# Kernel tuning notes

Hardware: AMD Instinct MI355X
Metric: run time of the kernel (lower is better)

## Reference

```python
import jax, jax.numpy as jnp
import numpy as np

N_PTS = 1048576
N_FEATS = 32
GRID = (96, 96, 96)
L = 6                      # num_positional_encoding_terms
D_IN = N_FEATS + 2 * L * 3  # 68
H_DIM = 128
VMIN, VMAX = -1.0, 1.0


def setup_inputs() -> dict:
    key = jax.random.key(0)
    ks = jax.random.split(key, 5)
    def lin(k, shp, fan):
        return jax.random.normal(k, shp, jnp.float32) * (1.0 / np.sqrt(fan).astype(np.float32))
    return {
        "x": jax.random.uniform(ks[0], (N_PTS, 3), jnp.float32),          # coords in [0,1) subset of [-1,1]
        "feature_grid": jax.random.uniform(ks[1], (1, N_FEATS) + GRID, jnp.float32),
        "W0": lin(ks[2], (H_DIM, D_IN), D_IN), "b0": jnp.zeros((H_DIM,), jnp.float32),
        "W1": lin(ks[3], (H_DIM, H_DIM), H_DIM), "b1": jnp.zeros((H_DIM,), jnp.float32),
        "W2": lin(ks[4], (1, H_DIM), H_DIM), "b2": jnp.zeros((1,), jnp.float32),
    }


def positional_encoding(x):
    # x: [N, d] -> [N, 2*L*d], NeRF-style: per frequency 2^i * pi, [sin | cos]
    freqs = jnp.pi * (2.0 ** jnp.arange(L, dtype=jnp.float32))   # [L]
    xf = x[:, None, :] * freqs[None, :, None]                    # [N, L, d]
    return jnp.concatenate([jnp.sin(xf), jnp.cos(xf)], axis=-1).reshape(x.shape[0], -1)


def grid_sample_3d(grid, coords):
    # Trilinear F.grid_sample, align_corners=True.
    # grid: [C, D, H, W]; coords: [N, 3] in [-1,1], ordered (x, y, z) -> (W, H, D)
    C, D, H, W = grid.shape
    def unnorm(c, size):
        return (c + 1.0) * 0.5 * (size - 1)
    fx, fy, fz = unnorm(coords[:, 0], W), unnorm(coords[:, 1], H), unnorm(coords[:, 2], D)
    x0, y0, z0 = jnp.floor(fx), jnp.floor(fy), jnp.floor(fz)
    wx, wy, wz = fx - x0, fy - y0, fz - z0
    def ci(i, size):
        return jnp.clip(i.astype(jnp.int32), 0, size - 1)
    x0i, x1i = ci(x0, W), ci(x0 + 1, W)
    y0i, y1i = ci(y0, H), ci(y0 + 1, H)
    z0i, z1i = ci(z0, D), ci(z0 + 1, D)
    def g(zi, yi, xi):
        return grid[:, zi, yi, xi]   # irregular gather -> [C, N]
    return (g(z0i, y0i, x0i) * ((1 - wz) * (1 - wy) * (1 - wx))
          + g(z0i, y0i, x1i) * ((1 - wz) * (1 - wy) * wx)
          + g(z0i, y1i, x0i) * ((1 - wz) * wy * (1 - wx))
          + g(z0i, y1i, x1i) * ((1 - wz) * wy * wx)
          + g(z1i, y0i, x0i) * (wz * (1 - wy) * (1 - wx))
          + g(z1i, y0i, x1i) * (wz * (1 - wy) * wx)
          + g(z1i, y1i, x0i) * (wz * wy * (1 - wx))
          + g(z1i, y1i, x1i) * (wz * wy * wx))   # [C, N]


def reference(x, feature_grid, W0, b0, W1, b1, W2, b2):
    feats = grid_sample_3d(feature_grid[0], x).T                       # [N, C]
    h = jnp.concatenate([positional_encoding(x), feats], axis=1)       # [N, 68]
    h = jax.nn.relu(h @ W0.T + b0)                                     # [N, 128]
    h = jax.nn.relu(h @ W1.T + b1)                                     # [N, 128]
    y = h @ W2.T + b2                                                  # [N, 1]
    return y * (VMAX - VMIN) + VMIN
```

## Files before the change

kernel.cpp:

```cpp
#include <hip/hip_runtime.h>

#define NPTS 1048576
#define NCH 32
#define GS 96
#define GV (GS * GS * GS)
#define DIN 68
#define HD 128
#define TILE_PTS 32
#define NTILES (NPTS / TILE_PTS)
#define NBLK 256
#define NTHR 768
#define WAVES_TOT (NBLK * 12)

typedef __bf16 bf16x8 __attribute__((ext_vector_type(8)));
typedef float f32x4 __attribute__((ext_vector_type(4)));
typedef float f32x2 __attribute__((ext_vector_type(2)));

__device__ __forceinline__ unsigned int f2bf(float f) {
  unsigned int u = __float_as_uint(f);
  return (u + 0x7fffu + ((u >> 16) & 1u)) >> 16;
}
__device__ __forceinline__ unsigned int pkbf(float a, float b) {
  return f2bf(a) | (f2bf(b) << 16);
}

__global__ __launch_bounds__(256) void k_prep_grid(const float* __restrict__ src,
                                                   unsigned int* __restrict__ dst) {
  __shared__ unsigned int tile[256 * 17];
  const int tid = threadIdx.x;
  const long vb = (long)blockIdx.x * 256;
  const int c2 = tid >> 4;
  const int vgb = tid & 15;
#pragma unroll
  for (int p = 0; p < 4; ++p) {
    int vox = (vgb + p * 16) * 4;
    const float4 a = *(const float4*)(src + (long)(2 * c2) * GV + vb + vox);
    const float4 b = *(const float4*)(src + (long)(2 * c2 + 1) * GV + vb + vox);
    tile[(vox + 0) * 17 + c2] = pkbf(a.x, b.x);
    tile[(vox + 1) * 17 + c2] = pkbf(a.y, b.y);
    tile[(vox + 2) * 17 + c2] = pkbf(a.z, b.z);
    tile[(vox + 3) * 17 + c2] = pkbf(a.w, b.w);
  }
  __syncthreads();
  const int vox2 = tid >> 2;
  const int c4 = (tid & 3) * 4;
#pragma unroll
  for (int j = 0; j < 4; ++j) {
    int vx = vox2 + j * 64;
    uint4 w;
    w.x = tile[vx * 17 + c4 + 0];
    w.y = tile[vx * 17 + c4 + 1];
    w.z = tile[vx * 17 + c4 + 2];
    w.w = tile[vx * 17 + c4 + 3];
    *(uint4*)(dst + (vb + vx) * 16 + c4) = w;
  }
}

template <bool TA>
__global__ __launch_bounds__(NTHR, 3) void k_fvsrn(
    const float* __restrict__ X, const float* __restrict__ gridF,
    const unsigned short* __restrict__ gridT,
    const float* __restrict__ W0, const float* __restrict__ B0,
    const float* __restrict__ W1, const float* __restrict__ B1,
    const float* __restrict__ W2, const float* __restrict__ B2,
    float* __restrict__ out) {
  extern __shared__ char smem[];
  float* lb0 = (float*)(smem + 57344);
  float* lb1 = (float*)(smem + 57856);
  float* lw2 = (float*)(smem + 58368);
  const int tid = threadIdx.x;

  for (int idx = tid; idx < 56 * 64; idx += NTHR) {
    int f = idx >> 6;
    int L = idx & 63;
    int qq = L >> 4, lnn = L & 15;
    float vals[8];
    if (f < 24) {
      int kt = f >> 3, nt = f & 7;
      int n = nt * 16 + lnn;
      int kb = kt * 32 + qq * 8;
#pragma unroll
      for (int j = 0; j < 8; ++j) {
        int k = kb + j;
        float w = 0.f;
        if (k < 32) w = W0[n * DIN + 36 + k];
        else if (k < DIN) w = W0[n * DIN + (k - 32)];
        vals[j] = w;
      }
    } else {
      int g = f - 24;
      int kt = g >> 3, nt = g & 7;
      int n = nt * 16 + lnn;
      int kb = kt * 32 + qq * 8;
#pragma unroll
      for (int j = 0; j < 8; ++j) vals[j] = W1[n * HD + kb + j];
    }
    uint4 pk;
    pk.x = pkbf(vals[0], vals[1]);
    pk.y = pkbf(vals[2], vals[3]);
    pk.z = pkbf(vals[4], vals[5]);
    pk.w = pkbf(vals[6], vals[7]);
    *(uint4*)(smem + f * 1024 + L * 16) = pk;
  }
  if (tid < 128) lb0[tid] = B0[tid];
  else if (tid < 256) lb1[tid - 128] = B1[tid - 128];
  else if (tid < 384) lw2[tid - 256] = W2[tid - 256];
  __syncthreads();

  const int wave = tid >> 6, lane = tid & 63;
  char* scr = smem + 58880 + wave * 8192;
  const int q = lane >> 4, ln = lane & 15;
  const int half = lane >> 5, pt = lane & 31;
  const int mtg = pt >> 4, pmg = pt & 15;
  const float b2s = B2[0];

  int t = blockIdx.x * 12 + wave;
  float px = 0.f, py = 0.f, pz = 0.f;
  if (t < NTILES) {
    long p = (long)t * TILE_PTS + pt;
    px = X[p * 3 + 0]; py = X[p * 3 + 1]; pz = X[p * 3 + 2];
  }

  for (; t < NTILES;) {
    const int tn = t + WAVES_TOT;
    const long p0 = (long)t * TILE_PTS;

    float v36[36];
    {
      const float PIf = 3.14159265358979f;
      float cc[3] = {px, py, pz};
#pragma unroll
      for (int ax = 0; ax < 3; ++ax) {
        float s, co;
        __sincosf(PIf * cc[ax], &s, &co);
#pragma unroll
        for (int i = 0; i < 6; ++i) {
          v36[i * 6 + ax] = s;
          v36[i * 6 + 3 + ax] = co;
          float s2 = 2.f * s * co;
          co = 1.f - 2.f * s * s;
          s = s2;
        }
      }
    }
    unsigned int pd[8], e0, e1;
    if (half == 0) {
#pragma unroll
      for (int d = 0; d < 8; ++d) pd[d] = pkbf(v36[2 * d], v36[2 * d + 1]);
      e0 = pkbf(v36[32], v36[33]);
      e1 = pkbf(v36[34], v36[35]);
    } else {
#pragma unroll
      for (int d = 0; d < 8; ++d) pd[d] = pkbf(v36[16 + 2 * d], v36[17 + 2 * d]);
      e0 = 0u; e1 = 0u;
    }

    f32x2 f2[8];
#pragma unroll
    for (int i = 0; i < 8; ++i) f2[i] = (f32x2){0.f, 0.f};
    {
      float fx = (px + 1.f) * 0.5f * (GS - 1);
      float fy = (py + 1.f) * 0.5f * (GS - 1);
      float fz = (pz + 1.f) * 0.5f * (GS - 1);
      float flx = floorf(fx), fly = floorf(fy), flz = floorf(fz);
      float wx = fx - flx, wy = fy - fly, wz = fz - flz;
      int jx = (int)flx, jy = (int)fly, jz = (int)flz;
      int ixa0 = min(max(jx, 0), GS - 1), ixa1 = min(max(jx + 1, 0), GS - 1);
      int iya0 = min(max(jy, 0), GS - 1), iya1 = min(max(jy + 1, 0), GS - 1);
      int iza0 = min(max(jz, 0), GS - 1), iza1 = min(max(jz + 1, 0), GS - 1);
#pragma unroll
      for (int zi = 0; zi < 2; ++zi) {
        int izz = zi ? iza1 : iza0;
        float wzz = zi ? wz : 1.f - wz;
#pragma unroll
        for (int yi = 0; yi < 2; ++yi) {
          int iyy = yi ? iya1 : iya0;
          float wyy = yi ? wy : 1.f - wy;
#pragma unroll
          for (int xi = 0; xi < 2; ++xi) {
            int ixx = xi ? ixa1 : ixa0;
            float w = wzz * wyy * (xi ? wx : 1.f - wx);
            f32x2 w2 = {w, w};
            long vi = ((long)izz * GS + iyy) * GS + ixx;
            if constexpr (TA) {
              const uint4* gp = (const uint4*)(gridT + vi * NCH + 16 * half);
              uint4 g0 = gp[0], g1 = gp[1];
#define ACC_PAIR(u, i)                                                     \
  {                                                                        \
    f32x2 u2 = {__uint_as_float((u) << 16),                                \
                __uint_as_float((u) & 0xffff0000u)};                       \
    f2[i] = __builtin_elementwise_fma(u2, w2, f2[i]);                      \
  }
              ACC_PAIR(g0.x, 0) ACC_PAIR(g0.y, 1) ACC_PAIR(g0.z, 2) ACC_PAIR(g0.w, 3)
              ACC_PAIR(g1.x, 4) ACC_PAIR(g1.y, 5) ACC_PAIR(g1.z, 6) ACC_PAIR(g1.w, 7)
#undef ACC_PAIR
            } else {
#pragma unroll
              for (int i = 0; i < 8; ++i) {
                int c = 16 * half + 2 * i;
                f32x2 u2 = {gridF[(long)c * GV + vi], gridF[(long)(c + 1) * GV + vi]};
                f2[i] = __builtin_elementwise_fma(u2, w2, f2[i]);
              }
            }
          }
        }
      }
    }

    {
      char* fbase = scr + (mtg * 3) * 1024;
      int ro = pmg * 16;
      uint4 s;
      s.x = pkbf(f2[0].x, f2[0].y); s.y = pkbf(f2[1].x, f2[1].y);
      s.z = pkbf(f2[2].x, f2[2].y); s.w = pkbf(f2[3].x, f2[3].y);
      *(uint4*)(fbase + (2 * half) * 256 + ro) = s;
      s.x = pkbf(f2[4].x, f2[4].y); s.y = pkbf(f2[5].x, f2[5].y);
      s.z = pkbf(f2[6].x, f2[6].y); s.w = pkbf(f2[7].x, f2[7].y);
      *(uint4*)(fbase + (2 * half + 1) * 256 + ro) = s;
      s.x = pd[0]; s.y = pd[1]; s.z = pd[2]; s.w = pd[3];
      *(uint4*)(fbase + 1024 + (2 * half) * 256 + ro) = s;
      s.x = pd[4]; s.y = pd[5]; s.z = pd[6]; s.w = pd[7];
      *(uint4*)(fbase + 1024 + (2 * half + 1) * 256 + ro) = s;
      s.x = e0; s.y = e1; s.z = 0u; s.w = 0u;
      *(uint4*)(fbase + 2048 + (2 * half) * 256 + ro) = s;
      s.x = 0u; s.y = 0u; s.z = 0u; s.w = 0u;
      *(uint4*)(fbase + 2048 + (2 * half + 1) * 256 + ro) = s;
    }
    __builtin_amdgcn_wave_barrier();

    if (tn < NTILES) {
      long p = (long)tn * TILE_PTS + pt;
      px = X[p * 3 + 0]; py = X[p * 3 + 1]; pz = X[p * 3 + 2];
    }

    bf16x8 a0[6];
#pragma unroll
    for (int mt = 0; mt < 2; ++mt)
#pragma unroll
      for (int kt = 0; kt < 3; ++kt)
        a0[mt * 3 + kt] = *(const bf16x8*)(scr + (mt * 3 + kt) * 1024 + lane * 16);
    __builtin_amdgcn_wave_barrier();
#pragma unroll
    for (int nt = 0; nt < 8; ++nt) {
      float bn = lb0[nt * 16 + ln];
      f32x4 cinit = {bn, bn, bn, bn};
      f32x4 acc[2];
      acc[0] = cinit; acc[1] = cinit;
#pragma unroll
      for (int kt = 0; kt < 3; ++kt) {
        bf16x8 bfr = *(const bf16x8*)(smem + (kt * 8 + nt) * 1024 + lane * 16);
#pragma unroll
        for (int mt = 0; mt < 2; ++mt)
          acc[mt] = __builtin_amdgcn_mfma_f32_16x16x32_bf16(a0[mt * 3 + kt], bfr, acc[mt], 0, 0, 0);
      }
      int n = nt * 16 + ln;
      int kt1 = n >> 5, j = n & 7, sub = (n >> 3) & 3;
#pragma unroll
      for (int mt = 0; mt < 2; ++mt)
#pragma unroll
        for (int r = 0; r < 4; ++r) {
          float h = fmaxf(acc[mt][r], 0.f);
          *(unsigned short*)(scr + (mt * 4 + kt1) * 1024 + (sub * 16 + q * 4 + r) * 16 + j * 2) =
              (unsigned short)f2bf(h);
        }
    }
    __builtin_amdgcn_wave_barrier();

    bf16x8 a1[8];
#pragma unroll
    for (int mt = 0; mt < 2; ++mt)
#pragma unroll
      for (int kt = 0; kt < 4; ++kt)
        a1[mt * 4 + kt] = *(const bf16x8*)(scr + (mt * 4 + kt) * 1024 + lane * 16);
    __builtin_amdgcn_wave_barrier();
    float y[8];
#pragma unroll
    for (int i = 0; i < 8; ++i) y[i] = 0.f;
#pragma unroll
    for (int nt = 0; nt < 8; ++nt) {
      float bn = lb1[nt * 16 + ln];
      float w2n = lw2[nt * 16 + ln];
      f32x4 cinit = {bn, bn, bn, bn};
      f32x4 acc[2];
      acc[0] = cinit; acc[1] = cinit;
#pragma unroll
      for (int kt = 0; kt < 4; ++kt) {
        bf16x8 bfr = *(const bf16x8*)(smem + 24576 + (kt * 8 + nt) * 1024 + lane * 16);
#pragma unroll
        for (int mt = 0; mt < 2; ++mt)
          acc[mt] = __builtin_amdgcn_mfma_f32_16x16x32_bf16(a1[mt * 4 + kt], bfr, acc[mt], 0, 0, 0);
      }
#pragma unroll
      for (int mt = 0; mt < 2; ++mt)
#pragma unroll
        for (int r = 0; r < 4; ++r)
          y[mt * 4 + r] += w2n * fmaxf(acc[mt][r], 0.f);
    }
#pragma unroll
    for (int i = 0; i < 8; ++i) {
      float v = y[i];
      v += __shfl_xor(v, 1);
      v += __shfl_xor(v, 2);
      v += __shfl_xor(v, 4);
      v += __shfl_xor(v, 8);
      y[i] = v;
    }
    if (ln == 0) {
#pragma unroll
      for (int mt = 0; mt < 2; ++mt)
#pragma unroll
        for (int r = 0; r < 4; ++r)
          out[p0 + mt * 16 + q * 4 + r] = (y[mt * 4 + r] + b2s) * 2.f - 1.f;
    }
    t = tn;
  }
}

extern "C" void kernel_launch(void* const* d_in, const int* in_sizes, int n_in,
                              void* d_out, int out_size, void* d_ws, size_t ws_size,
                              hipStream_t stream) {
  const float* X  = (const float*)d_in[0];
  const float* G  = (const float*)d_in[1];
  const float* W0 = (const float*)d_in[2];
  const float* B0 = (const float*)d_in[3];
  const float* W1 = (const float*)d_in[4];
  const float* B1 = (const float*)d_in[5];
  const float* W2 = (const float*)d_in[6];
  const float* B2 = (const float*)d_in[7];
  float* out = (float*)d_out;

  const size_t needT = (size_t)GV * NCH * 2;
  const size_t shmem = 157184;

  if (ws_size >= needT) {
    k_prep_grid<<<GV / 256, 256, 0, stream>>>(G, (unsigned int*)d_ws);
    k_fvsrn<true><<<NBLK, NTHR, shmem, stream>>>(
        X, G, (const unsigned short*)d_ws, W0, B0, W1, B1, W2, B2, out);
  } else {
    k_fvsrn<false><<<NBLK, NTHR, shmem, stream>>>(
        X, G, (const unsigned short*)nullptr, W0, B0, W1, B1, W2, B2, out);
  }
}
```

Before: 301.0 us.

## Prefetch next tile's grid corner gathers across MLP and use packed bf16 convert

Issues the eight trilinear corner gathers for the next tile into 16 uint4 registers before the current tile's MLP runs, so gather latency overlaps the MFMA work. It also loads the next coordinates earlier, uses 32-bit index arithmetic, and switches bf16 packing to a hardware packed-convert builtin when one is available, packing two ReLU outputs per convert. The cost is 64 more live VGPRs, which may lower occupancy. The initial coordinate load also loses its bounds check.

```diff
diff --git a/kernel.cpp b/kernel.cpp
--- a/kernel.cpp
+++ b/kernel.cpp
@@ -21,7 +21,11 @@
   return (u + 0x7fffu + ((u >> 16) & 1u)) >> 16;
 }
 __device__ __forceinline__ unsigned int pkbf(float a, float b) {
+#if __has_builtin(__builtin_amdgcn_cvt_pk_bf16_f32)
+  return __builtin_bit_cast(unsigned int, __builtin_amdgcn_cvt_pk_bf16_f32(a, b));
+#else
   return f2bf(a) | (f2bf(b) << 16);
+#endif
 }
 
 __global__ __launch_bounds__(256) void k_prep_grid(const float* __restrict__ src,
@@ -115,15 +119,48 @@
   const float b2s = B2[0];
 
   int t = blockIdx.x * 12 + wave;
-  float px = 0.f, py = 0.f, pz = 0.f;
-  if (t < NTILES) {
-    long p = (long)t * TILE_PTS + pt;
-    px = X[p * 3 + 0]; py = X[p * 3 + 1]; pz = X[p * 3 + 2];
-  }
+  unsigned p3 = ((unsigned)t * TILE_PTS + pt) * 3u;
+  float px = X[p3], py = X[p3 + 1], pz = X[p3 + 2];
+
+  uint4 cg[16];
+
+  auto corner_issue = [&](float cx, float cy, float cz) {
+    float fx = (cx + 1.f) * 0.5f * (GS - 1);
+    float fy = (cy + 1.f) * 0.5f * (GS - 1);
+    float fz = (cz + 1.f) * 0.5f * (GS - 1);
+    int jx = (int)floorf(fx), jy = (int)floorf(fy), jz = (int)floorf(fz);
+    int ix0 = min(max(jx, 0), GS - 1), ix1 = min(max(jx + 1, 0), GS - 1);
+    int iy0 = min(max(jy, 0), GS - 1), iy1 = min(max(jy + 1, 0), GS - 1);
+    int iz0 = min(max(jz, 0), GS - 1), iz1 = min(max(jz + 1, 0), GS - 1);
+    unsigned zy[4];
+    zy[0] = ((unsigned)(iz0 * GS + iy0)) * GS;
+    zy[1] = ((unsigned)(iz0 * GS + iy1)) * GS;
+    zy[2] = ((unsigned)(iz1 * GS + iy0)) * GS;
+    zy[3] = ((unsigned)(iz1 * GS + iy1)) * GS;
+    unsigned hb = (unsigned)(half << 4);
+#pragma unroll
+    for (int c = 0; c < 4; ++c) {
+      unsigned o0 = ((zy[c] + (unsigned)ix0) << 5) + hb;
+      unsigned o1 = ((zy[c] + (unsigned)ix1) << 5) + hb;
+      const uint4* g0 = (const uint4*)(gridT + o0);
+      const uint4* g1 = (const uint4*)(gridT + o1);
+      cg[4 * c + 0] = g0[0];
+      cg[4 * c + 1] = g0[1];
+      cg[4 * c + 2] = g1[0];
+      cg[4 * c + 3] = g1[1];
+    }
+  };
+  if constexpr (TA) corner_issue(px, py, pz);
 
   for (; t < NTILES;) {
     const int tn = t + WAVES_TOT;
-    const long p0 = (long)t * TILE_PTS;
+    const unsigned p0 = (unsigned)t * TILE_PTS;
+
+    float nx = px, ny = py, nz = pz;
+    if (tn < NTILES) {
+      unsigned np3 = ((unsigned)tn * TILE_PTS + pt) * 3u;
+      nx = X[np3]; ny = X[np3 + 1]; nz = X[np3 + 2];
+    }
 
     float v36[36];
     {
@@ -162,49 +199,52 @@
       float fx = (px + 1.f) * 0.5f * (GS - 1);
       float fy = (py + 1.f) * 0.5f * (GS - 1);
       float fz = (pz + 1.f) * 0.5f * (GS - 1);
-      float flx = floorf(fx), fly = floorf(fy), flz = floorf(fz);
-      float wx = fx - flx, wy = fy - fly, wz = fz - flz;
-      int jx = (int)flx, jy = (int)fly, jz = (int)flz;
-      int ixa0 = min(max(jx, 0), GS - 1), ixa1 = min(max(jx + 1, 0), GS - 1);
-      int iya0 = min(max(jy, 0), GS - 1), iya1 = min(max(jy + 1, 0), GS - 1);
-      int iza0 = min(max(jz, 0), GS - 1), iza1 = min(max(jz + 1, 0), GS - 1);
-#pragma unroll
-      for (int zi = 0; zi < 2; ++zi) {
-        int izz = zi ? iza1 : iza0;
-        float wzz = zi ? wz : 1.f - wz;
-#pragma unroll
-        for (int yi = 0; yi < 2; ++yi) {
-          int iyy = yi ? iya1 : iya0;
-          float wyy = yi ? wy : 1.f - wy;
-#pragma unroll
-          for (int xi = 0; xi < 2; ++xi) {
-            int ixx = xi ? ixa1 : ixa0;
-            float w = wzz * wyy * (xi ? wx : 1.f - wx);
-            f32x2 w2 = {w, w};
-            long vi = ((long)izz * GS + iyy) * GS + ixx;
-            if constexpr (TA) {
-              const uint4* gp = (const uint4*)(gridT + vi * NCH + 16 * half);
-              uint4 g0 = gp[0], g1 = gp[1];
+      float wx = fx - floorf(fx), wy = fy - floorf(fy), wz = fz - floorf(fz);
+      float wxa[2] = {1.f - wx, wx};
+      float wya[2] = {1.f - wy, wy};
+      float wza[2] = {1.f - wz, wz};
+      if constexpr (TA) {
+#pragma unroll
+        for (int c = 0; c < 8; ++c) {
+          int zi = c >> 2, yi = (c >> 1) & 1, xi = c & 1;
+          float w = wza[zi] * wya[yi] * wxa[xi];
+          f32x2 w2 = {w, w};
+          uint4 g0 = cg[4 * (zi * 2 + yi) + xi * 2 + 0];
+          uint4 g1 = cg[4 * (zi * 2 + yi) + xi * 2 + 1];
 #define ACC_PAIR(u, i)                                                     \
   {                                                                        \
     f32x2 u2 = {__uint_as_float((u) << 16),                                \
                 __uint_as_float((u) & 0xffff0000u)};                       \
     f2[i] = __builtin_elementwise_fma(u2, w2, f2[i]);                      \
   }
-              ACC_PAIR(g0.x, 0) ACC_PAIR(g0.y, 1) ACC_PAIR(g0.z, 2) ACC_PAIR(g0.w, 3)
-              ACC_PAIR(g1.x, 4) ACC_PAIR(g1.y, 5) ACC_PAIR(g1.z, 6) ACC_PAIR(g1.w, 7)
+          ACC_PAIR(g0.x, 0) ACC_PAIR(g0.y, 1) ACC_PAIR(g0.z, 2) ACC_PAIR(g0.w, 3)
+          ACC_PAIR(g1.x, 4) ACC_PAIR(g1.y, 5) ACC_PAIR(g1.z, 6) ACC_PAIR(g1.w, 7)
 #undef ACC_PAIR
-            } else {
-#pragma unroll
-              for (int i = 0; i < 8; ++i) {
-                int c = 16 * half + 2 * i;
-                f32x2 u2 = {gridF[(long)c * GV + vi], gridF[(long)(c + 1) * GV + vi]};
-                f2[i] = __builtin_elementwise_fma(u2, w2, f2[i]);
-              }
-            }
+        }
+      } else {
+        int jx = (int)floorf(fx), jy = (int)floorf(fy), jz = (int)floorf(fz);
+        int ix0 = min(max(jx, 0), GS - 1), ix1 = min(max(jx + 1, 0), GS - 1);
+        int iy0 = min(max(jy, 0), GS - 1), iy1 = min(max(jy + 1, 0), GS - 1);
+        int iz0 = min(max(jz, 0), GS - 1), iz1 = min(max(jz + 1, 0), GS - 1);
+        int ixa[2] = {ix0, ix1}, iya[2] = {iy0, iy1}, iza[2] = {iz0, iz1};
+#pragma unroll
+        for (int c = 0; c < 8; ++c) {
+          int zi = c >> 2, yi = (c >> 1) & 1, xi = c & 1;
+          float w = wza[zi] * wya[yi] * wxa[xi];
+          f32x2 w2 = {w, w};
+          long vi = ((long)iza[zi] * GS + iya[yi]) * GS + ixa[xi];
+#pragma unroll
+          for (int i = 0; i < 8; ++i) {
+            int ch = 16 * half + 2 * i;
+            f32x2 u2 = {gridF[(long)ch * GV + vi], gridF[(long)(ch + 1) * GV + vi]};
+            f2[i] = __builtin_elementwise_fma(u2, w2, f2[i]);
           }
         }
       }
+    }
+
+    if constexpr (TA) {
+      if (tn < NTILES) corner_issue(nx, ny, nz);
     }
 
     {
@@ -228,11 +268,6 @@
     }
     __builtin_amdgcn_wave_barrier();
 
-    if (tn < NTILES) {
-      long p = (long)tn * TILE_PTS + pt;
-      px = X[p * 3 + 0]; py = X[p * 3 + 1]; pz = X[p * 3 + 2];
-    }
-
     bf16x8 a0[6];
 #pragma unroll
     for (int mt = 0; mt < 2; ++mt)
@@ -258,10 +293,11 @@
 #pragma unroll
       for (int mt = 0; mt < 2; ++mt)
 #pragma unroll
-        for (int r = 0; r < 4; ++r) {
-          float h = fmaxf(acc[mt][r], 0.f);
-          *(unsigned short*)(scr + (mt * 4 + kt1) * 1024 + (sub * 16 + q * 4 + r) * 16 + j * 2) =
-              (unsigned short)f2bf(h);
+        for (int r = 0; r < 4; r += 2) {
+          unsigned pk2 = pkbf(fmaxf(acc[mt][r], 0.f), fmaxf(acc[mt][r + 1], 0.f));
+          char* ba = scr + (mt * 4 + kt1) * 1024 + j * 2;
+          *(unsigned short*)(ba + (sub * 16 + q * 4 + r) * 16) = (unsigned short)pk2;
+          *(unsigned short*)(ba + (sub * 16 + q * 4 + r + 1) * 16) = (unsigned short)(pk2 >> 16);
         }
     }
     __builtin_amdgcn_wave_barrier();
@@ -312,6 +348,7 @@
         for (int r = 0; r < 4; ++r)
           out[p0 + mt * 16 + q * 4 + r] = (y[mt * 4 + r] + b2s) * 2.f - 1.f;
     }
+    px = nx; py = ny; pz = nz;
     t = tn;
   }
 }
```

After: 445.6 us. 1.48x slower.
